# Kernel tuning notes

Measured on AMD Instinct MI355X. Metric: run time of the kernel, lower is better.

The kernel has to match this reference:

```python
import jax, jax.numpy as jnp
import numpy as np

LN_EPS = 1e-3  # keras LayerNormalization default epsilon


def _prefix_weights(S, dtype):
    # W[i, j] = 1/(i-j)^2 for j < i, else 0  (distance = i - j)
    idx = jnp.arange(S)
    diff = idx[:, None] - idx[None, :]
    safe = jnp.where(diff > 0, diff, 1).astype(dtype)
    return jnp.where(diff > 0, 1.0 / (safe * safe), jnp.zeros((), dtype))


def setup_inputs() -> dict:
    key = jax.random.key(0)
    k1, k2 = jax.random.split(key)
    B, S, E = 2, 512, 256
    x = jax.random.normal(k1, (B, S, E), dtype=jnp.float32)
    concept_map = jax.random.normal(k2, (E, E, E), dtype=jnp.float32) * 0.02
    gamma = jnp.ones((E,), dtype=jnp.float32)
    beta = jnp.zeros((E,), dtype=jnp.float32)
    return {"x": x, "concept_map": concept_map, "gamma": gamma, "beta": beta}


def reference(x, concept_map, gamma, beta):
    B, S, E = x.shape
    # positional-weighted prefix sum: s[b,i,:] = sum_{j<i} x[b,j,:] / (i-j)^2
    W = _prefix_weights(S, x.dtype)            # (S, S) lower-triangular
    s = jnp.einsum('ij,bjd->bid', W, x)        # (B, S, E)
    # outer product x_i (x) s_i contracted with cubic concept_map:
    # result[b,i,c] = sum_{a,p} x[b,i,a] * s[b,i,p] * concept_map[c,a,p]
    # (stacked conceptual_matrices broadcast against concept_map, summed over
    #  the last two axes -- equivalent bilinear contraction)
    y = jnp.einsum('bsa,bsp,cap->bsc', x, s, concept_map)
    y = y + x  # residual
    # LayerNormalization over last axis (keras defaults: eps=1e-3, affine)
    mean = jnp.mean(y, axis=-1, keepdims=True)
    var = jnp.mean(jnp.square(y - mean), axis=-1, keepdims=True)
    y = (y - mean) * jax.lax.rsqrt(var + LN_EPS) * gamma + beta
    # Dropout is identity at inference
    return y
```

## Files before the change

### kernel.cpp

```cpp
#include <hip/hip_runtime.h>
#include <hip/hip_fp16.h>
#include <cstdint>

#define BB 2
#define SS 512
#define EE 256
#define NN (BB*SS)
#define KTOT (EE*EE)
#define SPLITK 32
#define KCHUNK (KTOT/SPLITK)
#define NSTEP (KCHUNK/32)
#define TSTEPS (KTOT/32)
#define LN_EPS 1e-3f

typedef _Float16 f16;
typedef _Float16 f16x8 __attribute__((ext_vector_type(8)));
typedef float    f32x4 __attribute__((ext_vector_type(4)));

__global__ void prep_kernel(const float* __restrict__ cm, f16* __restrict__ cmP,
                            const float* __restrict__ x, float* __restrict__ ps) {
    __shared__ float xt[64][128];
    __shared__ float wl2[576];
    const int bid = blockIdx.x;
    const int tid = threadIdx.x;

    if (bid < TSTEPS) {
        const int t    = bid;
        const int slot = tid >> 6;
        const int cq   = (tid & 63) * 4;
        const float* src = cm + (size_t)t * 32 + slot * 8;
        f16* dst = cmP + (size_t)t * 8192 + tid * 32;
        #pragma unroll
        for (int u = 0; u < 4; ++u) {
            const float* row = src + (size_t)(cq + u) * KTOT;
            float4 lo = *(const float4*)(row);
            float4 hi = *(const float4*)(row + 4);
            f16x8 h = { (f16)lo.x, (f16)lo.y, (f16)lo.z, (f16)lo.w,
                        (f16)hi.x, (f16)hi.y, (f16)hi.z, (f16)hi.w };
            *(f16x8*)(dst + u * 8) = h;
        }
        return;
    }

    const int id = bid - TSTEPS;
    const int eh = id & 1;
    const int rest = id >> 1;
    const int b = rest / 36;
    const int r = rest % 36;
    int it = 0;
    while ((it + 1) * (it + 2) / 2 <= r) ++it;
    const int jt = r - it * (it + 1) / 2;

    for (int t = tid; t < 576; t += 256) {
        const int d = t - 64;
        wl2[t] = (d > 0) ? 1.0f / ((float)d * (float)d) : 0.0f;
    }
    const int jbase = jt * 64, ibase = it * 64;
    const float* xb = x + ((size_t)b * SS + jbase) * EE + eh * 128;
    #pragma unroll
    for (int p = 0; p < 8; ++p) {
        const int row = p * 8 + (tid >> 5);
        const int col = (tid & 31) * 4;
        *(float4*)&xt[row][col] = *(const float4*)(xb + (size_t)row * EE + col);
    }
    __syncthreads();

    const int g  = tid >> 5;
    const int ec = (tid & 31) * 4;
    const int irow = ibase + g * 8;
    float4 acc[8];
    #pragma unroll
    for (int m = 0; m < 8; ++m) acc[m] = (float4){0.f, 0.f, 0.f, 0.f};

    for (int jj = 0; jj < 64; ++jj) {
        const float4 xv = *(const float4*)&xt[jj][ec];
        const int wbase = irow - (jbase + jj) + 64;
        #pragma unroll
        for (int m = 0; m < 8; ++m) {
            const float w = wl2[wbase + m];
            acc[m].x += xv.x * w;
            acc[m].y += xv.y * w;
            acc[m].z += xv.z * w;
            acc[m].w += xv.w * w;
        }
    }

    float* base = ps + ((size_t)(((b * 2 + eh) * 8 + it) * 8 + jt)) * (64 * 128);
    #pragma unroll
    for (int m = 0; m < 8; ++m)
        *(float4*)(base + (size_t)(g * 8 + m) * 128 + ec) = acc[m];
}

__global__ void reduce_s_kernel(const float* __restrict__ ps, float* __restrict__ s) {
    const int n = blockIdx.x;
    const int e = threadIdx.x;
    const int b = n >> 9, i = n & (SS - 1);
    const int it = i >> 6, il = i & 63;
    const int eh = e >> 7, ec = e & 127;
    const size_t tbase = (size_t)((b * 2 + eh) * 8 + it) * 8;
    float acc = 0.0f;
    for (int jt = 0; jt <= it; ++jt)
        acc += ps[(tbase + jt) * (64 * 128) + (size_t)il * 128 + ec];
    s[(size_t)n * EE + e] = acc;
}

__launch_bounds__(256, 2)
__global__ void gemm_kernel(const float* __restrict__ x,
                            const float* __restrict__ sbuf,
                            const f16* __restrict__ cmP,
                            float* __restrict__ part) {
    __shared__ __align__(16) f16 Bs[4][8192];
    const int tid  = threadIdx.x;
    const int lane = tid & 63;
    const int wave = tid >> 6;
    const int koct = lane >> 4;
    const int cl   = lane & 15;

    const int d = blockIdx.x;
    const int nblock = (d >> 3) & 15;
    const int chunk  = (d & 7) * 4 + (d >> 7);

    f16x8 xf[4];
    #pragma unroll
    for (int rt = 0; rt < 4; ++rt) {
        const int r = nblock * 64 + rt * 16 + cl;
        const float* xr = x + (size_t)r * EE + chunk * 8;
        float4 xlo = *(const float4*)(xr);
        float4 xhi = *(const float4*)(xr + 4);
        xf[rt] = (f16x8){ (f16)xlo.x, (f16)xlo.y, (f16)xlo.z, (f16)xlo.w,
                          (f16)xhi.x, (f16)xhi.y, (f16)xhi.z, (f16)xhi.w };
    }
    float4 p0[4][2];
    #pragma unroll
    for (int rt = 0; rt < 4; ++rt) {
        const int r = nblock * 64 + rt * 16 + cl;
        const float* sr = sbuf + (size_t)r * EE + koct * 8;
        p0[rt][0] = *(const float4*)(sr);
        p0[rt][1] = *(const float4*)(sr + 4);
    }
    __builtin_amdgcn_sched_barrier(0);

    f32x4 acc[4][4];
    #pragma unroll
    for (int a = 0; a < 4; ++a)
        #pragma unroll
        for (int b = 0; b < 4; ++b) acc[a][b] = (f32x4){0.f, 0.f, 0.f, 0.f};

    const char* srcBase = (const char*)cmP + (size_t)(chunk * NSTEP) * 16384;
    auto stageV = [&](int v) {
        const int t = ((v & 7) << 3) | (v >> 3);
        const char* g = srcBase + (size_t)t * 16384 + wave * 1024 + lane * 16;
        char* l = (char*)&Bs[v & 3][0] + wave * 1024;
        #pragma unroll
        for (int i = 0; i < 4; ++i) {
            __builtin_amdgcn_global_load_lds(
                (const __attribute__((address_space(1))) void*)(g + i * 4096),
                (__attribute__((address_space(3))) void*)(l + i * 4096),
                16, 0, 0);
        }
    };

    stageV(0); stageV(1); stageV(2);
    asm volatile("s_waitcnt vmcnt(8)" ::: "memory");
    __builtin_amdgcn_sched_barrier(0);

    f16x8 svm[4];
    #pragma unroll
    for (int rt = 0; rt < 4; ++rt)
        svm[rt] = (f16x8){ (f16)p0[rt][0].x, (f16)p0[rt][0].y,
                           (f16)p0[rt][0].z, (f16)p0[rt][0].w,
                           (f16)p0[rt][1].x, (f16)p0[rt][1].y,
                           (f16)p0[rt][1].z, (f16)p0[rt][1].w };

    const int cb = koct * 2048 + (wave * 64 + cl) * 8;

    f16x8 bfc[4], afc[4];
    {
        const f16* bb = &Bs[0][cb];
        #pragma unroll
        for (int ct = 0; ct < 4; ++ct) bfc[ct] = *(const f16x8*)(bb + ct * 128);
        #pragma unroll
        for (int rt = 0; rt < 4; ++rt) {
            const f16 xa = xf[rt][0];
            const f16x8 xa8 = { xa, xa, xa, xa, xa, xa, xa, xa };
            afc[rt] = xa8 * svm[rt];
        }
    }

    #pragma unroll
    for (int m = 0; m < 8; ++m) {
        float4 pnxt[4][2];
        #pragma unroll
        for (int a_l = 0; a_l < 8; ++a_l) {
            const int v = m * 8 + a_l;

            if (a_l == 6 && m < 7) {
                #pragma unroll
                for (int rt = 0; rt < 4; ++rt) {
                    const int r = nblock * 64 + rt * 16 + cl;
                    const float* sr = sbuf + (size_t)r * EE + (m + 1) * 32 + koct * 8;
                    pnxt[rt][0] = *(const float4*)(sr);
                    pnxt[rt][1] = *(const float4*)(sr + 4);
                }
                __builtin_amdgcn_sched_barrier(0);
            }

            __builtin_amdgcn_s_setprio(1);
            #pragma unroll
            for (int ct = 0; ct < 4; ++ct)
                #pragma unroll
                for (int rt = 0; rt < 4; ++rt)
                    acc[rt][ct] = __builtin_amdgcn_mfma_f32_16x16x32_f16(afc[rt], bfc[ct], acc[rt][ct], 0, 0, 0);
            __builtin_amdgcn_s_setprio(0);

            if (v + 3 < NSTEP) stageV(v + 3);

            if (v <= 60) {
                if (a_l == 6 && m < 7) asm volatile("s_waitcnt vmcnt(16)" ::: "memory");
                else                   asm volatile("s_waitcnt vmcnt(8)"  ::: "memory");
            } else if (v == 61)        asm volatile("s_waitcnt vmcnt(4)"  ::: "memory");
            else if (v == 62)          asm volatile("s_waitcnt vmcnt(0)"  ::: "memory");
            __builtin_amdgcn_sched_barrier(0);

            if (v < 63) {
                const f16* bb = &Bs[0][0] + (size_t)((v + 1) & 3) * 8192 + cb;
                f16x8 bfn[4];
                #pragma unroll
                for (int ct = 0; ct < 4; ++ct) bfn[ct] = *(const f16x8*)(bb + ct * 128);
                if (a_l == 7) {
                    #pragma unroll
                    for (int rt = 0; rt < 4; ++rt)
                        svm[rt] = (f16x8){ (f16)pnxt[rt][0].x, (f16)pnxt[rt][0].y,
                                           (f16)pnxt[rt][0].z, (f16)pnxt[rt][0].w,
                                           (f16)pnxt[rt][1].x, (f16)pnxt[rt][1].y,
                                           (f16)pnxt[rt][1].z, (f16)pnxt[rt][1].w };
                }
                #pragma unroll
                for (int rt = 0; rt < 4; ++rt) {
                    const f16 xa = xf[rt][(a_l + 1) & 7];
                    const f16x8 xa8 = { xa, xa, xa, xa, xa, xa, xa, xa };
                    const f16x8 afn = xa8 * svm[rt];
                    afc[rt] = afn;
                }
                #pragma unroll
                for (int ct = 0; ct < 4; ++ct) bfc[ct] = bfn[ct];
                __builtin_amdgcn_sched_barrier(0);
            }
        }
    }

    #pragma unroll
    for (int rt = 0; rt < 4; ++rt) {
        #pragma unroll
        for (int ct = 0; ct < 4; ++ct) {
            const int c  = wave * 64 + ct * 16 + cl;
            const int rb = nblock * 64 + rt * 16 + koct * 4;
            #pragma unroll
            for (int q = 0; q < 4; ++q)
                part[((size_t)chunk * NN + rb + q) * EE + c] = acc[rt][ct][q];
        }
    }
}

__global__ void reduce_ln_kernel(const float* __restrict__ x,
                                 const float* __restrict__ part,
                                 const float* __restrict__ gamma,
                                 const float* __restrict__ beta,
                                 float* __restrict__ out) {
    const int n = blockIdx.x;
    const int c = threadIdx.x;
    const int lane = c & 63, wave = c >> 6;
    float y = x[(size_t)n * EE + c];
    #pragma unroll 8
    for (int ch = 0; ch < SPLITK; ++ch)
        y += part[((size_t)ch * NN + n) * EE + c];

    float v = y;
    #pragma unroll
    for (int o = 32; o > 0; o >>= 1) v += __shfl_xor(v, o);
    __shared__ float red[8];
    if (lane == 0) red[wave] = v;
    __syncthreads();
    const float mean = (red[0] + red[1] + red[2] + red[3]) * (1.0f / EE);
    const float d = y - mean;
    float sq = d * d;
    #pragma unroll
    for (int o = 32; o > 0; o >>= 1) sq += __shfl_xor(sq, o);
    if (lane == 0) red[4 + wave] = sq;
    __syncthreads();
    const float var = (red[4] + red[5] + red[6] + red[7]) * (1.0f / EE);
    out[(size_t)n * EE + c] = d * rsqrtf(var + LN_EPS) * gamma[c] + beta[c];
}

extern "C" void kernel_launch(void* const* d_in, const int* in_sizes, int n_in,
                              void* d_out, int out_size, void* d_ws, size_t ws_size,
                              hipStream_t stream) {
    const float* x     = (const float*)d_in[0];
    const float* cm    = (const float*)d_in[1];
    const float* gamma = (const float*)d_in[2];
    const float* beta  = (const float*)d_in[3];
    float* out = (float*)d_out;

    float* sbuf = (float*)d_ws;
    f16*   cmP  = (f16*)(sbuf + (size_t)NN * EE);
    float* part = (float*)((char*)cmP + (size_t)TSTEPS * 8192 * sizeof(f16));
    float* ps   = part;

    hipLaunchKernelGGL(prep_kernel, dim3(TSTEPS + 144), dim3(256), 0, stream,
                       cm, cmP, x, ps);
    hipLaunchKernelGGL(reduce_s_kernel, dim3(NN), dim3(256), 0, stream, ps, sbuf);
    hipLaunchKernelGGL(gemm_kernel, dim3(16 * SPLITK), dim3(256), 0, stream,
                       x, sbuf, cmP, part);
    hipLaunchKernelGGL(reduce_ln_kernel, dim3(NN), dim3(256), 0, stream,
                       x, part, gamma, beta, out);
}
```

Measured before the change: 81.90 us.

## Coalesce concept_map packing via LDS transpose and store split-K partials as fp16

The concept_map fp32-to-fp16 packing is restructured: each block now reads contiguous 512-element row segments of concept_map, transposes them through shared memory, and writes packed tiles. This replaces strided gathers and cuts the number of pack blocks. The GEMM epilogue stages its accumulators in shared memory and writes split-K partials as fp16 with 16-byte coalesced stores, which halves partial traffic for both the GEMM and the LayerNorm reduction. Storing partials in fp16 adds rounding error across 32 summed chunks.

After: 75.19 us. 1.09x faster.

```diff
diff --git a/kernel.cpp b/kernel.cpp
--- a/kernel.cpp
+++ b/kernel.cpp
@@ -17,32 +17,52 @@
 typedef _Float16 f16x8 __attribute__((ext_vector_type(8)));
 typedef float    f32x4 __attribute__((ext_vector_type(4)));
 
+#define NPACK 512
+
 __global__ void prep_kernel(const float* __restrict__ cm, f16* __restrict__ cmP,
                             const float* __restrict__ x, float* __restrict__ ps) {
-    __shared__ float xt[64][128];
-    __shared__ float wl2[576];
+    __shared__ __align__(16) char smem[35072];
     const int bid = blockIdx.x;
     const int tid = threadIdx.x;
-
-    if (bid < TSTEPS) {
-        const int t    = bid;
-        const int slot = tid >> 6;
-        const int cq   = (tid & 63) * 4;
-        const float* src = cm + (size_t)t * 32 + slot * 8;
-        f16* dst = cmP + (size_t)t * 8192 + tid * 32;
-        #pragma unroll
-        for (int u = 0; u < 4; ++u) {
-            const float* row = src + (size_t)(cq + u) * KTOT;
-            float4 lo = *(const float4*)(row);
-            float4 hi = *(const float4*)(row + 4);
-            f16x8 h = { (f16)lo.x, (f16)lo.y, (f16)lo.z, (f16)lo.w,
-                        (f16)hi.x, (f16)hi.y, (f16)hi.z, (f16)hi.w };
-            *(f16x8*)(dst + u * 8) = h;
+    const int wave = tid >> 6;
+    const int lane = tid & 63;
+
+    if (bid < NPACK) {
+        const int cg = bid >> 7;
+        const int kg = bid & 127;
+        f16* lt = (f16*)smem;
+        #pragma unroll
+        for (int h = 0; h < 2; ++h) {
+            #pragma unroll
+            for (int i = 0; i < 8; ++i) {
+                const int rl = i * 4 + wave;
+                const int row = cg * 64 + h * 32 + rl;
+                const float* src = cm + (size_t)row * KTOT + kg * 512 + lane * 8;
+                float4 lo = *(const float4*)(src);
+                float4 hi = *(const float4*)(src + 4);
+                f16x8 v = { (f16)lo.x, (f16)lo.y, (f16)lo.z, (f16)lo.w,
+                            (f16)hi.x, (f16)hi.y, (f16)hi.z, (f16)hi.w };
+                *(f16x8*)(lt + lane * 264 + rl * 8) = v;
+            }
+            __syncthreads();
+            #pragma unroll
+            for (int jj = 0; jj < 8; ++jj) {
+                const int s  = jj * 8 + wave * 2 + (lane >> 5);
+                const int cl = lane & 31;
+                f16x8 v = *(const f16x8*)(lt + s * 264 + cl * 8);
+                const int t    = kg * 16 + (s >> 2);
+                const int koct = s & 3;
+                const int c    = cg * 64 + h * 32 + cl;
+                *(f16x8*)(cmP + (size_t)t * 8192 + koct * 2048 + c * 8) = v;
+            }
+            __syncthreads();
         }
         return;
     }
 
-    const int id = bid - TSTEPS;
+    float (*xt)[128] = (float(*)[128])smem;
+    float* wl2 = (float*)(smem + 32768);
+    const int id = bid - NPACK;
     const int eh = id & 1;
     const int rest = id >> 1;
     const int b = rest / 36;
@@ -108,7 +128,7 @@
 __global__ void gemm_kernel(const float* __restrict__ x,
                             const float* __restrict__ sbuf,
                             const f16* __restrict__ cmP,
-                            float* __restrict__ part) {
+                            f16* __restrict__ part) {
     __shared__ __align__(16) f16 Bs[4][8192];
     const int tid  = threadIdx.x;
     const int lane = tid & 63;
@@ -239,8 +259,7 @@
                 for (int rt = 0; rt < 4; ++rt) {
                     const f16 xa = xf[rt][(a_l + 1) & 7];
                     const f16x8 xa8 = { xa, xa, xa, xa, xa, xa, xa, xa };
-                    const f16x8 afn = xa8 * svm[rt];
-                    afc[rt] = afn;
+                    afc[rt] = xa8 * svm[rt];
                 }
                 #pragma unroll
                 for (int ct = 0; ct < 4; ++ct) bfc[ct] = bfn[ct];
@@ -249,21 +268,34 @@
         }
     }
 
+    __syncthreads();
+    f16* Ep = (f16*)&Bs[0][0];
     #pragma unroll
     for (int rt = 0; rt < 4; ++rt) {
         #pragma unroll
         for (int ct = 0; ct < 4; ++ct) {
-            const int c  = wave * 64 + ct * 16 + cl;
-            const int rb = nblock * 64 + rt * 16 + koct * 4;
+            const int col = wave * 64 + ct * 16 + cl;
             #pragma unroll
-            for (int q = 0; q < 4; ++q)
-                part[((size_t)chunk * NN + rb + q) * EE + c] = acc[rt][ct][q];
-        }
+            for (int q = 0; q < 4; ++q) {
+                const int lr = rt * 16 + koct * 4 + q;
+                Ep[lr * 264 + col] = (f16)acc[rt][ct][q];
+            }
+        }
+    }
+    __syncthreads();
+    {
+        const int lr  = tid >> 2;
+        const int seg = tid & 3;
+        f16* dst = part + ((size_t)chunk * NN + nblock * 64 + lr) * EE + seg * 64;
+        const f16* srcE = Ep + lr * 264 + seg * 64;
+        #pragma unroll
+        for (int i = 0; i < 8; ++i)
+            *(f16x8*)(dst + i * 8) = *(const f16x8*)(srcE + i * 8);
     }
 }
 
 __global__ void reduce_ln_kernel(const float* __restrict__ x,
-                                 const float* __restrict__ part,
+                                 const f16* __restrict__ part,
                                  const float* __restrict__ gamma,
                                  const float* __restrict__ beta,
                                  float* __restrict__ out) {
@@ -273,7 +305,7 @@
     float y = x[(size_t)n * EE + c];
     #pragma unroll 8
     for (int ch = 0; ch < SPLITK; ++ch)
-        y += part[((size_t)ch * NN + n) * EE + c];
+        y += (float)part[((size_t)ch * NN + n) * EE + c];
 
     float v = y;
     #pragma unroll
@@ -303,10 +335,10 @@
 
     float* sbuf = (float*)d_ws;
     f16*   cmP  = (f16*)(sbuf + (size_t)NN * EE);
-    float* part = (float*)((char*)cmP + (size_t)TSTEPS * 8192 * sizeof(f16));
-    float* ps   = part;
-
-    hipLaunchKernelGGL(prep_kernel, dim3(TSTEPS + 144), dim3(256), 0, stream,
+    f16*   part = (f16*)((char*)cmP + (size_t)TSTEPS * 8192 * sizeof(f16));
+    float* ps   = (float*)part;
+
+    hipLaunchKernelGGL(prep_kernel, dim3(NPACK + 144), dim3(256), 0, stream,
                        cm, cmP, x, ps);
     hipLaunchKernelGGL(reduce_s_kernel, dim3(NN), dim3(256), 0, stream, ps, sbuf);
     hipLaunchKernelGGL(gemm_kernel, dim3(16 * SPLITK), dim3(256), 0, stream,
```
